# Kernel tuning notes

Measured on AMD Instinct MI355X. Metric: run time of the kernel, lower is better.

The kernel has to match this reference:

```python
import jax, jax.numpy as jnp
import numpy as np

B, G, K = 16, 5000, 256
NUM_CELLS, HID = 100, 64
STEPS, ALPHA = 10, 0.1


def setup_inputs() -> dict:
    key = jax.random.key(0)
    ks = jax.random.split(key, 10)
    ctl = jax.random.normal(ks[0], (B, G), dtype=jnp.float32)
    drug_targets = jax.random.uniform(ks[1], (B, G), dtype=jnp.float32)
    cell_idx = jax.random.randint(ks[2], (B,), 0, NUM_CELLS)
    drug_fp = jax.random.normal(ks[3], (B, 128), dtype=jnp.float32)
    # gene->module membership matrix (constructor constant M_gk)
    M = jax.random.uniform(ks[4], (G, K), dtype=jnp.float32)
    # module-module adjacency (constructor constant A_kk), column-normalized for stability
    A = jax.random.uniform(ks[5], (K, K), dtype=jnp.float32)
    A = A / jnp.sum(A, axis=0, keepdims=True)
    # shared Dense(hidden_dim, relu): input feature dim is 3 (ctl, t, z_gene stacked)
    W1 = jax.random.normal(ks[6], (3, HID), dtype=jnp.float32) * 0.5
    b1 = jnp.zeros((HID,), dtype=jnp.float32)
    cell_emb = jax.random.normal(ks[7], (NUM_CELLS, HID), dtype=jnp.float32) * 0.05
    W2 = jax.random.normal(ks[8], (HID, 1), dtype=jnp.float32) * 0.1
    b2 = jnp.zeros((1,), dtype=jnp.float32)
    return {"ctl": ctl, "drug_targets": drug_targets, "cell_idx": cell_idx,
            "drug_fp": drug_fp, "M": M, "A": A, "W1": W1, "b1": b1,
            "cell_emb": cell_emb, "W2": W2, "b2": b2}


def reference(ctl, drug_targets, cell_idx, drug_fp, M, A, W1, b1, cell_emb, W2, b2):
    t = drug_targets                                   # [B, G]
    # max-pool gene targets into modules: max_g t[b,g] * M[g,k]
    t_mod = jnp.max(t[:, :, None] * M[None, :, :], axis=1)   # [B, K]
    # APPNP propagation: Z = (1-alpha) * Z @ A + alpha * S, fixed 10 steps
    Z = t_mod
    for _ in range(STEPS):
        Z = (1.0 - ALPHA) * (Z @ A) + ALPHA * t_mod
    z_gene = Z @ M.T                                   # [B, G]
    x = jnp.stack([ctl, t, z_gene], axis=-1)           # [B, G, 3]
    h = jax.nn.relu(x @ W1 + b1)                       # [B, G, HID]
    h = h + cell_emb[cell_idx][:, None, :]             # broadcast cell embedding
    y = jnp.squeeze(h @ W2 + b2, axis=-1)              # [B, G]
    return y
```

## Files before the change

kernel.cpp:

```cpp
#include <hip/hip_runtime.h>

#define G 5000
#define K 256
#define BATCH 16
#define HID 64
#define STEPS 10
#define NC 250
#define GPER 20

__global__ void maxpool_kernel(const float* __restrict__ t,
                               const float* __restrict__ M,
                               const float* __restrict__ A,
                               float* __restrict__ partials,
                               float* __restrict__ awarm) {
    __shared__ float tl[GPER][BATCH];
    const int c  = blockIdx.x;
    const int k  = threadIdx.x;
    const int g0 = c * GPER;

    float4 aw = make_float4(0.f, 0.f, 0.f, 0.f);
    if (k < 64)
        aw = ((const float4*)A)[((size_t)blockIdx.x * 64 + k) & 16383];

    for (int i = k; i < GPER * BATCH; i += 256) {
        int gi = i >> 4, b = i & 15;
        tl[gi][b] = t[b * G + g0 + gi];
    }
    __syncthreads();

    float mx[BATCH];
#pragma unroll
    for (int b = 0; b < BATCH; ++b) mx[b] = 0.f;

#pragma unroll 4
    for (int gi = 0; gi < GPER; ++gi) {
        float mg = M[(size_t)(g0 + gi) * K + k];
#pragma unroll
        for (int b = 0; b < BATCH; ++b)
            mx[b] = fmaxf(mx[b], tl[gi][b] * mg);
    }
#pragma unroll
    for (int b = 0; b < BATCH; ++b)
        partials[((size_t)c * BATCH + b) * K + k] = mx[b];

    if (k < 64) awarm[k] = aw.x + aw.y + aw.z + aw.w;
}

__global__ __launch_bounds__(1024, 4)
void appnp_fused(const float* __restrict__ partials,
                 const float* __restrict__ A,
                 const int* __restrict__ cell_idx,
                 const float* __restrict__ cell_emb,
                 const float* __restrict__ W2,
                 const float* __restrict__ b2,
                 float* __restrict__ Zfin,
                 float* __restrict__ ce_dot) {
    __shared__ float4 zb[2][K / 4];
    __shared__ float  Sm[K];
    __shared__ float  red[4][K];
    __shared__ float  ce_red[HID];

    const int b  = blockIdx.x;
    const int t  = threadIdx.x;
    const int k  = t & 255;
    const int jc = t >> 8;
    const int j0 = jc * 64;

    float Areg[64];
#pragma unroll
    for (int jj = 0; jj < 64; ++jj)
        Areg[jj] = A[(size_t)(j0 + jj) * K + k];

    {
        const int CPJ = (NC + 3) / 4;
        int c0 = jc * CPJ, c1 = min(NC, c0 + CPJ);
        float m = 0.f;
        for (int c = c0; c < c1; ++c)
            m = fmaxf(m, partials[((size_t)c * BATCH + b) * K + k]);
        red[jc][k] = m;
    }
    if (t < HID) {
        int ci = cell_idx[b];
        ce_red[t] = cell_emb[ci * HID + t] * W2[t];
    }
    __syncthreads();
    if (jc == 0) {
        float s = fmaxf(fmaxf(red[0][k], red[1][k]), fmaxf(red[2][k], red[3][k]));
        Sm[k] = s;
        ((float*)zb)[k] = s;
    }
    if (t == 0) {
        float s = b2[0];
        for (int h = 0; h < HID; ++h) s += ce_red[h];
        ce_dot[b] = s;
    }
    __syncthreads();

    for (int s = 0; s < STEPS; ++s) {
        const float4* cur4 = zb[s & 1] + (j0 >> 2);
        float*        nxt  = (float*)zb[(s + 1) & 1];
        float acc = 0.f;
#pragma unroll
        for (int q = 0; q < 16; ++q) {
            float4 c4 = cur4[q];
            acc = fmaf(c4.x, Areg[4 * q + 0], acc);
            acc = fmaf(c4.y, Areg[4 * q + 1], acc);
            acc = fmaf(c4.z, Areg[4 * q + 2], acc);
            acc = fmaf(c4.w, Areg[4 * q + 3], acc);
        }
        red[jc][k] = acc;
        __syncthreads();
        if (jc == 0)
            nxt[k] = 0.9f * (red[0][k] + red[1][k] + red[2][k] + red[3][k])
                   + 0.1f * Sm[k];
        __syncthreads();
    }
    if (jc == 0) Zfin[b * K + k] = ((float*)zb)[k];
}

__global__ void final_kernel(const float* __restrict__ ctl,
                             const float* __restrict__ t_in,
                             const float* __restrict__ Z,
                             const float* __restrict__ M,
                             const float* __restrict__ W1,
                             const float* __restrict__ b1,
                             const float* __restrict__ W2,
                             const float* __restrict__ ce_dot,
                             float* __restrict__ out) {
    __shared__ float4 wpack[HID];
    __shared__ float  w2l[HID];
    __shared__ float  cel[BATCH];

    const int t = threadIdx.x;
    if (t < HID) {
        wpack[t] = make_float4(W1[t], W1[HID + t], W1[2 * HID + t], b1[t]);
        w2l[t] = W2[t];
    }
    if (t < BATCH) cel[t] = ce_dot[t];
    __syncthreads();

    const int gl = t & 63;
    const int bg = __builtin_amdgcn_readfirstlane(t >> 6);
    const int g  = blockIdx.x * 64 + gl;
    if (g >= G) return;

    const float4* Zw = (const float4*)(Z + (size_t)bg * 4 * K);

    float acc[4] = {0.f, 0.f, 0.f, 0.f};
    const float4* M4 = (const float4*)(M + (size_t)g * K);
#pragma unroll 4
    for (int k4 = 0; k4 < K / 4; ++k4) {
        float4 m4 = M4[k4];
#pragma unroll
        for (int i = 0; i < 4; ++i) {
            float4 z4 = Zw[i * (K / 4) + k4];
            acc[i] = fmaf(m4.x, z4.x, acc[i]);
            acc[i] = fmaf(m4.y, z4.y, acc[i]);
            acc[i] = fmaf(m4.z, z4.z, acc[i]);
            acc[i] = fmaf(m4.w, z4.w, acc[i]);
        }
    }

    float cv[4], tv[4], y[4];
#pragma unroll
    for (int i = 0; i < 4; ++i) {
        int b = bg * 4 + i;
        cv[i] = ctl[b * G + g];
        tv[i] = t_in[b * G + g];
        y[i] = cel[b];
    }
#pragma unroll 4
    for (int h = 0; h < HID; ++h) {
        float4 w = wpack[h];
        float w2h = w2l[h];
#pragma unroll
        for (int i = 0; i < 4; ++i) {
            float pre = w.w;
            pre = fmaf(cv[i], w.x, pre);
            pre = fmaf(tv[i], w.y, pre);
            pre = fmaf(acc[i], w.z, pre);
            pre = fmaxf(pre, 0.f);
            y[i] = fmaf(pre, w2h, y[i]);
        }
    }
#pragma unroll
    for (int i = 0; i < 4; ++i)
        out[(bg * 4 + i) * G + g] = y[i];
}

extern "C" void kernel_launch(void* const* d_in, const int* in_sizes, int n_in,
                              void* d_out, int out_size, void* d_ws, size_t ws_size,
                              hipStream_t stream) {
    const float* ctl      = (const float*)d_in[0];
    const float* tgt      = (const float*)d_in[1];
    const int*   cell_idx = (const int*)d_in[2];
    const float* M        = (const float*)d_in[4];
    const float* A        = (const float*)d_in[5];
    const float* W1       = (const float*)d_in[6];
    const float* b1       = (const float*)d_in[7];
    const float* cell_emb = (const float*)d_in[8];
    const float* W2       = (const float*)d_in[9];
    const float* b2       = (const float*)d_in[10];
    float* out = (float*)d_out;

    float* partials = (float*)d_ws;
    float* Zfin  = partials + (size_t)NC * BATCH * K;
    float* ce    = Zfin + BATCH * K;
    float* awarm = ce + BATCH;

    maxpool_kernel<<<NC, 256, 0, stream>>>(tgt, M, A, partials, awarm);
    appnp_fused<<<BATCH, 1024, 0, stream>>>(partials, A, cell_idx, cell_emb,
                                            W2, b2, Zfin, ce);
    final_kernel<<<(G + 63) / 64, 256, 0, stream>>>(ctl, tgt, Zfin, M, W1, b1,
                                                    W2, ce, out);
}
```

Baseline: 121.1 us.

## Halve maxpool chunks, vectorize partial reduction, stage Z in shared memory

The maxpool stage now gives each block 40 genes instead of 20, so it emits half as many partial rows. The APPNP kernel reduces those partials with float4 loads across 16 chunk groups and then does a 16-way max in shared memory. The final kernel copies the whole Z matrix into LDS once per block and reads it there instead of through uniform global loads. In exchange, maxpool runs fewer blocks with longer loops, and the final kernel pays an extra LDS fill and sync per block.

```diff
diff --git a/kernel.cpp b/kernel.cpp
--- a/kernel.cpp
+++ b/kernel.cpp
@@ -5,8 +5,8 @@
 #define BATCH 16
 #define HID 64
 #define STEPS 10
-#define NC 250
-#define GPER 20
+#define NC 125
+#define GPER 40
 
 __global__ void maxpool_kernel(const float* __restrict__ t,
                                const float* __restrict__ M,
@@ -19,8 +19,8 @@
     const int g0 = c * GPER;
 
     float4 aw = make_float4(0.f, 0.f, 0.f, 0.f);
-    if (k < 64)
-        aw = ((const float4*)A)[((size_t)blockIdx.x * 64 + k) & 16383];
+    if (k < 128)
+        aw = ((const float4*)A)[((size_t)blockIdx.x * 128 + k) & 16383];
 
     for (int i = k; i < GPER * BATCH; i += 256) {
         int gi = i >> 4, b = i & 15;
@@ -43,7 +43,7 @@
     for (int b = 0; b < BATCH; ++b)
         partials[((size_t)c * BATCH + b) * K + k] = mx[b];
 
-    if (k < 64) awarm[k] = aw.x + aw.y + aw.z + aw.w;
+    if (k < 128) awarm[k & 63] = aw.x + aw.y + aw.z + aw.w;
 }
 
 __global__ __launch_bounds__(1024, 4)
@@ -57,7 +57,7 @@
                  float* __restrict__ ce_dot) {
     __shared__ float4 zb[2][K / 4];
     __shared__ float  Sm[K];
-    __shared__ float  red[4][K];
+    __shared__ float  red[16][K];
     __shared__ float  ce_red[HID];
 
     const int b  = blockIdx.x;
@@ -72,12 +72,18 @@
         Areg[jj] = A[(size_t)(j0 + jj) * K + k];
 
     {
-        const int CPJ = (NC + 3) / 4;
-        int c0 = jc * CPJ, c1 = min(NC, c0 + CPJ);
-        float m = 0.f;
-        for (int c = c0; c < c1; ++c)
-            m = fmaxf(m, partials[((size_t)c * BATCH + b) * K + k]);
-        red[jc][k] = m;
+        const int k4 = t & 63;
+        const int cg = t >> 6;
+        const float4* p4 = (const float4*)partials;
+        float4 m4 = make_float4(0.f, 0.f, 0.f, 0.f);
+        for (int c = cg; c < NC; c += 16) {
+            float4 v = p4[((size_t)c * BATCH + b) * (K / 4) + k4];
+            m4.x = fmaxf(m4.x, v.x);
+            m4.y = fmaxf(m4.y, v.y);
+            m4.z = fmaxf(m4.z, v.z);
+            m4.w = fmaxf(m4.w, v.w);
+        }
+        ((float4*)red[cg])[k4] = m4;
     }
     if (t < HID) {
         int ci = cell_idx[b];
@@ -85,7 +91,9 @@
     }
     __syncthreads();
     if (jc == 0) {
-        float s = fmaxf(fmaxf(red[0][k], red[1][k]), fmaxf(red[2][k], red[3][k]));
+        float s = red[0][k];
+#pragma unroll
+        for (int cgi = 1; cgi < 16; ++cgi) s = fmaxf(s, red[cgi][k]);
         Sm[k] = s;
         ((float*)zb)[k] = s;
     }
@@ -127,11 +135,14 @@
                              const float* __restrict__ W2,
                              const float* __restrict__ ce_dot,
                              float* __restrict__ out) {
+    __shared__ float4 zl[BATCH * (K / 4)];
     __shared__ float4 wpack[HID];
     __shared__ float  w2l[HID];
     __shared__ float  cel[BATCH];
 
     const int t = threadIdx.x;
+    const float4* Z4 = (const float4*)Z;
+    for (int i = t; i < BATCH * (K / 4); i += 256) zl[i] = Z4[i];
     if (t < HID) {
         wpack[t] = make_float4(W1[t], W1[HID + t], W1[2 * HID + t], b1[t]);
         w2l[t] = W2[t];
@@ -140,11 +151,9 @@
     __syncthreads();
 
     const int gl = t & 63;
-    const int bg = __builtin_amdgcn_readfirstlane(t >> 6);
-    const int g  = blockIdx.x * 64 + gl;
+    const int bg = t >> 6;
+    const int g = blockIdx.x * 64 + gl;
     if (g >= G) return;
-
-    const float4* Zw = (const float4*)(Z + (size_t)bg * 4 * K);
 
     float acc[4] = {0.f, 0.f, 0.f, 0.f};
     const float4* M4 = (const float4*)(M + (size_t)g * K);
@@ -153,7 +162,7 @@
         float4 m4 = M4[k4];
 #pragma unroll
         for (int i = 0; i < 4; ++i) {
-            float4 z4 = Zw[i * (K / 4) + k4];
+            float4 z4 = zl[(bg * 4 + i) * (K / 4) + k4];
             acc[i] = fmaf(m4.x, z4.x, acc[i]);
             acc[i] = fmaf(m4.y, z4.y, acc[i]);
             acc[i] = fmaf(m4.z, z4.z, acc[i]);
```

Measured after the change: 114.8 us. -5.2%, faster.
